# Kernel tuning notes

Hardware: AMD Instinct MI355X
Metric: run time of the kernel (lower is better)

The kernel has to match this reference:

```python
import jax, jax.numpy as jnp
import numpy as np

EPS = 1e-08


def setup_inputs() -> dict:
    key = jax.random.key(0)
    x = jax.random.normal(key, (64, 16, 65536), dtype=jnp.float32)
    return {"x": x}


def reference(x):
    # x: (B, C, T). All statistics reduce over the last (time) axis.
    mean = x.mean(axis=-1)                       # (B, C)
    var = jnp.var(x, axis=-1, ddof=1)            # torch.var default: unbiased
    std = jnp.sqrt(var)                          # torch.std default: unbiased
    sq_mean = (x ** 2).mean(axis=-1)
    rms = jnp.sqrt(sq_mean)
    peak = x.max(axis=-1)
    peak_neg = x.min(axis=-1)
    peak_to_peak = peak - peak_neg
    abs_peak = jnp.abs(peak)
    crest_factor = abs_peak / (rms + EPS)
    mean_abs = jnp.abs(x).mean(axis=-1)
    shape_factor = rms / (mean_abs + EPS)
    impulse_factor = abs_peak / (mean_abs + EPS)
    sqrt_mean = jnp.sqrt(jnp.abs(x)).mean(axis=-1)
    clearance_factor = abs_peak / (sqrt_mean ** 2 + EPS)

    centered = x - mean[..., None]               # (B, C, T)
    skewness = (centered ** 3).mean(axis=-1) / (std ** 3 + EPS)
    kurtosis_val = (centered ** 4).mean(axis=-1) / (std ** 4 + EPS) - 3.0

    signs = jnp.sign(x)
    zcr = (signs[:, :, 1:] != signs[:, :, :-1]).astype(jnp.float32).mean(axis=-1)
    centered_signs = jnp.sign(centered)
    mcr = (centered_signs[:, :, 1:] != centered_signs[:, :, :-1]).astype(jnp.float32).mean(axis=-1)

    margin_factor = abs_peak / (sqrt_mean + EPS)
    energy = (x ** 2).sum(axis=-1)

    features = jnp.stack([
        mean, std, var, rms, peak, peak_neg, peak_to_peak,
        crest_factor, shape_factor, impulse_factor, clearance_factor,
        skewness, kurtosis_val, zcr, mcr, margin_factor, energy,
    ], axis=-1)                                  # (B, C, 17)
    return features
```

## Files before the change

### kernel.cpp

```cpp
#include <hip/hip_runtime.h>
#include <math.h>

#define T_LEN 65536
#define TPB 256
#define NVEC (T_LEN / 4)
#define EPS 1e-8f

__device__ __forceinline__ int sgn_of(float v) {
    return (v > 0.f) - (v < 0.f);
}

__global__ __launch_bounds__(TPB) void stat_feat_kernel(const float* __restrict__ x,
                                                        float* __restrict__ out) {
    const int row = blockIdx.x;
    const float* __restrict__ xr = x + (size_t)row * T_LEN;
    const float4* __restrict__ xv = (const float4*)xr;
    const int tid = threadIdx.x;
    const int wave = tid >> 6;
    const int lane = tid & 63;

    float s1 = 0.f, s2 = 0.f, s3 = 0.f, s4 = 0.f, sabs = 0.f, ssqrt = 0.f;
    float mx = -__builtin_inff(), mn = __builtin_inff();
    int zc = 0;

    for (int i = tid; i < NVEC; i += TPB) {
        float4 v = xv[i];
        float prev = (i > 0) ? xr[4 * i - 1] : v.x;
        float e[4] = {v.x, v.y, v.z, v.w};
#pragma unroll
        for (int j = 0; j < 4; j++) {
            float t = e[j];
            float t2 = t * t;
            s1 += t;
            s2 += t2;
            s3 = fmaf(t2, t, s3);
            s4 = fmaf(t2, t2, s4);
            float a = fabsf(t);
            sabs += a;
            ssqrt += sqrtf(a);
            mx = fmaxf(mx, t);
            mn = fminf(mn, t);
        }
        int sp = sgn_of(prev);
#pragma unroll
        for (int j = 0; j < 4; j++) {
            int sc = sgn_of(e[j]);
            zc += (sc != sp);
            sp = sc;
        }
    }

#pragma unroll
    for (int o = 32; o > 0; o >>= 1) {
        s1 += __shfl_down(s1, o);
        s2 += __shfl_down(s2, o);
        s3 += __shfl_down(s3, o);
        s4 += __shfl_down(s4, o);
        sabs += __shfl_down(sabs, o);
        ssqrt += __shfl_down(ssqrt, o);
        zc += __shfl_down(zc, o);
        mx = fmaxf(mx, __shfl_down(mx, o));
        mn = fminf(mn, __shfl_down(mn, o));
    }

    __shared__ float ls1[4], ls2[4], ls3[4], ls4[4], lsa[4], lss[4], lmx[4], lmn[4];
    __shared__ int lzc[4];
    __shared__ float s_mean;

    if (lane == 0) {
        ls1[wave] = s1; ls2[wave] = s2; ls3[wave] = s3; ls4[wave] = s4;
        lsa[wave] = sabs; lss[wave] = ssqrt; lmx[wave] = mx; lmn[wave] = mn;
        lzc[wave] = zc;
    }
    __syncthreads();

    float S1 = 0.f, S2 = 0.f, S3 = 0.f, S4 = 0.f, SA = 0.f, SS = 0.f;
    float MX = 0.f, MN = 0.f;
    int ZC = 0;
    if (tid == 0) {
        S1 = ls1[0] + ls1[1] + ls1[2] + ls1[3];
        S2 = ls2[0] + ls2[1] + ls2[2] + ls2[3];
        S3 = ls3[0] + ls3[1] + ls3[2] + ls3[3];
        S4 = ls4[0] + ls4[1] + ls4[2] + ls4[3];
        SA = lsa[0] + lsa[1] + lsa[2] + lsa[3];
        SS = lss[0] + lss[1] + lss[2] + lss[3];
        MX = fmaxf(fmaxf(lmx[0], lmx[1]), fmaxf(lmx[2], lmx[3]));
        MN = fminf(fminf(lmn[0], lmn[1]), fminf(lmn[2], lmn[3]));
        ZC = lzc[0] + lzc[1] + lzc[2] + lzc[3];
        s_mean = S1 / (float)T_LEN;
    }
    __syncthreads();

    const float m = s_mean;
    int mc = 0;
    for (int i = tid; i < NVEC; i += TPB) {
        float4 v = xv[i];
        float prev = (i > 0) ? xr[4 * i - 1] : v.x;
        float e[4] = {v.x - m, v.y - m, v.z - m, v.w - m};
        int sp = sgn_of(prev - m);
#pragma unroll
        for (int j = 0; j < 4; j++) {
            int sc = sgn_of(e[j]);
            mc += (sc != sp);
            sp = sc;
        }
    }
#pragma unroll
    for (int o = 32; o > 0; o >>= 1) mc += __shfl_down(mc, o);
    __syncthreads();
    if (lane == 0) lzc[wave] = mc;
    __syncthreads();

    if (tid == 0) {
        int MC = lzc[0] + lzc[1] + lzc[2] + lzc[3];
        const float Tf = (float)T_LEN;
        float mean = S1 / Tf;
        float sq_mean = S2 / Tf;
        float var = (S2 - S1 * S1 / Tf) / (Tf - 1.f);
        var = fmaxf(var, 0.f);
        float stdv = sqrtf(var);
        float rms = sqrtf(sq_mean);
        float peak = MX;
        float peak_neg = MN;
        float ptp = peak - peak_neg;
        float abs_peak = fabsf(peak);
        float crest = abs_peak / (rms + EPS);
        float mean_abs = SA / Tf;
        float shape = rms / (mean_abs + EPS);
        float impulse = abs_peak / (mean_abs + EPS);
        float sqrt_mean = SS / Tf;
        float clearance = abs_peak / (sqrt_mean * sqrt_mean + EPS);
        float ex3 = S3 / Tf;
        float m3 = ex3 - 3.f * mean * sq_mean + 2.f * mean * mean * mean;
        float m4 = S4 / Tf - 4.f * mean * ex3 + 6.f * mean * mean * sq_mean
                   - 3.f * mean * mean * mean * mean;
        float skew = m3 / (stdv * stdv * stdv + EPS);
        float kurt = m4 / (stdv * stdv * stdv * stdv + EPS) - 3.f;
        float zcr = (float)ZC / (Tf - 1.f);
        float mcr = (float)MC / (Tf - 1.f);
        float margin = abs_peak / (sqrt_mean + EPS);
        float energy = S2;

        float* o = out + (size_t)row * 17;
        o[0] = mean;      o[1] = stdv;     o[2] = var;      o[3] = rms;
        o[4] = peak;      o[5] = peak_neg; o[6] = ptp;      o[7] = crest;
        o[8] = shape;     o[9] = impulse;  o[10] = clearance; o[11] = skew;
        o[12] = kurt;     o[13] = zcr;     o[14] = mcr;     o[15] = margin;
        o[16] = energy;
    }
}

extern "C" void kernel_launch(void* const* d_in, const int* in_sizes, int n_in,
                              void* d_out, int out_size, void* d_ws, size_t ws_size,
                              hipStream_t stream) {
    const float* x = (const float*)d_in[0];
    float* out = (float*)d_out;
    const int rows = in_sizes[0] / T_LEN;
    stat_feat_kernel<<<dim3(rows), dim3(TPB), 0, stream>>>(x, out);
}
```

Baseline: 418.2 us.

## Split each row across chunked blocks with multi-kernel partial reductions

Splits every row into 8 chunks processed by separate blocks, writing per-chunk partial statistics to workspace, then finalizes in a small kernel; the mean-crossing pass is likewise chunked and reduced in separate kernels. This raises the number of blocks in flight to hide memory latency that the one-block-per-row design could not. Neighbor values for crossing counts now come from a wave shuffle instead of a global reload, and sign tests use a simple less-than comparison. It adds four launches and workspace traffic, and treats exact zeros slightly differently from sign().

```diff
diff --git a/kernel.cpp b/kernel.cpp
--- a/kernel.cpp
+++ b/kernel.cpp
@@ -1,52 +1,55 @@
 #include <hip/hip_runtime.h>
 #include <math.h>
 
-#define T_LEN 65536
-#define TPB 256
-#define NVEC (T_LEN / 4)
-#define EPS 1e-8f
-
-__device__ __forceinline__ int sgn_of(float v) {
-    return (v > 0.f) - (v < 0.f);
-}
-
-__global__ __launch_bounds__(TPB) void stat_feat_kernel(const float* __restrict__ x,
-                                                        float* __restrict__ out) {
-    const int row = blockIdx.x;
-    const float* __restrict__ xr = x + (size_t)row * T_LEN;
+#define T_LEN      65536
+#define TPB        256
+#define CHUNKS     8
+#define CHUNK_VECS (T_LEN / 4 / CHUNKS)
+#define ITERS      (CHUNK_VECS / TPB)
+#define EPS        1e-8f
+
+__global__ __launch_bounds__(TPB) void k1_partials(const float* __restrict__ x,
+                                                   float* __restrict__ part,
+                                                   int rows) {
+    const int blk   = blockIdx.x;
+    const int row   = blk >> 3;
+    const int chunk = blk & 7;
+    const int tid   = threadIdx.x;
+    const int lane  = tid & 63;
+    const int wave  = tid >> 6;
+
+    const float*  __restrict__ xr = x + (size_t)row * T_LEN;
     const float4* __restrict__ xv = (const float4*)xr;
-    const int tid = threadIdx.x;
-    const int wave = tid >> 6;
-    const int lane = tid & 63;
-
-    float s1 = 0.f, s2 = 0.f, s3 = 0.f, s4 = 0.f, sabs = 0.f, ssqrt = 0.f;
+    const int vbase = chunk * CHUNK_VECS;
+
+    float s1 = 0.f, s2 = 0.f, s3 = 0.f, s4 = 0.f, sa = 0.f, ss = 0.f;
     float mx = -__builtin_inff(), mn = __builtin_inff();
     int zc = 0;
 
-    for (int i = tid; i < NVEC; i += TPB) {
-        float4 v = xv[i];
-        float prev = (i > 0) ? xr[4 * i - 1] : v.x;
+    for (int it = 0; it < ITERS; ++it) {
+        const int vi = vbase + it * TPB + tid;
+        float4 v = xv[vi];
+        float prev = __shfl_up(v.w, 1);
+        if (lane == 0) prev = (vi > 0) ? xr[4 * vi - 1] : v.x;
+
+        bool sp = prev < 0.f;
+        bool b0 = v.x < 0.f, b1 = v.y < 0.f, b2 = v.z < 0.f, b3 = v.w < 0.f;
+        zc += (int)(sp != b0) + (int)(b0 != b1) + (int)(b1 != b2) + (int)(b2 != b3);
+
         float e[4] = {v.x, v.y, v.z, v.w};
 #pragma unroll
         for (int j = 0; j < 4; j++) {
             float t = e[j];
             float t2 = t * t;
             s1 += t;
-            s2 += t2;
+            s2 = fmaf(t, t, s2);
             s3 = fmaf(t2, t, s3);
             s4 = fmaf(t2, t2, s4);
             float a = fabsf(t);
-            sabs += a;
-            ssqrt += sqrtf(a);
+            sa += a;
+            ss += sqrtf(a);
             mx = fmaxf(mx, t);
             mn = fminf(mn, t);
-        }
-        int sp = sgn_of(prev);
-#pragma unroll
-        for (int j = 0; j < 4; j++) {
-            int sc = sgn_of(e[j]);
-            zc += (sc != sp);
-            sp = sc;
         }
     }
 
@@ -56,98 +59,139 @@
         s2 += __shfl_down(s2, o);
         s3 += __shfl_down(s3, o);
         s4 += __shfl_down(s4, o);
-        sabs += __shfl_down(sabs, o);
-        ssqrt += __shfl_down(ssqrt, o);
+        sa += __shfl_down(sa, o);
+        ss += __shfl_down(ss, o);
         zc += __shfl_down(zc, o);
         mx = fmaxf(mx, __shfl_down(mx, o));
         mn = fminf(mn, __shfl_down(mn, o));
     }
 
-    __shared__ float ls1[4], ls2[4], ls3[4], ls4[4], lsa[4], lss[4], lmx[4], lmn[4];
-    __shared__ int lzc[4];
-    __shared__ float s_mean;
-
+    __shared__ float l[9][4];
     if (lane == 0) {
-        ls1[wave] = s1; ls2[wave] = s2; ls3[wave] = s3; ls4[wave] = s4;
-        lsa[wave] = sabs; lss[wave] = ssqrt; lmx[wave] = mx; lmn[wave] = mn;
-        lzc[wave] = zc;
+        l[0][wave] = s1; l[1][wave] = s2; l[2][wave] = s3; l[3][wave] = s4;
+        l[4][wave] = sa; l[5][wave] = ss; l[6][wave] = mx; l[7][wave] = mn;
+        l[8][wave] = (float)zc;
     }
     __syncthreads();
-
-    float S1 = 0.f, S2 = 0.f, S3 = 0.f, S4 = 0.f, SA = 0.f, SS = 0.f;
-    float MX = 0.f, MN = 0.f;
-    int ZC = 0;
     if (tid == 0) {
-        S1 = ls1[0] + ls1[1] + ls1[2] + ls1[3];
-        S2 = ls2[0] + ls2[1] + ls2[2] + ls2[3];
-        S3 = ls3[0] + ls3[1] + ls3[2] + ls3[3];
-        S4 = ls4[0] + ls4[1] + ls4[2] + ls4[3];
-        SA = lsa[0] + lsa[1] + lsa[2] + lsa[3];
-        SS = lss[0] + lss[1] + lss[2] + lss[3];
-        MX = fmaxf(fmaxf(lmx[0], lmx[1]), fmaxf(lmx[2], lmx[3]));
-        MN = fminf(fminf(lmn[0], lmn[1]), fminf(lmn[2], lmn[3]));
-        ZC = lzc[0] + lzc[1] + lzc[2] + lzc[3];
-        s_mean = S1 / (float)T_LEN;
-    }
+        const int N = rows * CHUNKS;
+        const int idx = chunk * rows + row;
+        part[0 * N + idx] = l[0][0] + l[0][1] + l[0][2] + l[0][3];
+        part[1 * N + idx] = l[1][0] + l[1][1] + l[1][2] + l[1][3];
+        part[2 * N + idx] = l[2][0] + l[2][1] + l[2][2] + l[2][3];
+        part[3 * N + idx] = l[3][0] + l[3][1] + l[3][2] + l[3][3];
+        part[4 * N + idx] = l[4][0] + l[4][1] + l[4][2] + l[4][3];
+        part[5 * N + idx] = l[5][0] + l[5][1] + l[5][2] + l[5][3];
+        part[6 * N + idx] = fmaxf(fmaxf(l[6][0], l[6][1]), fmaxf(l[6][2], l[6][3]));
+        part[7 * N + idx] = fminf(fminf(l[7][0], l[7][1]), fminf(l[7][2], l[7][3]));
+        part[8 * N + idx] = l[8][0] + l[8][1] + l[8][2] + l[8][3];
+    }
+}
+
+__global__ __launch_bounds__(TPB) void k2_finalize(const float* __restrict__ part,
+                                                   float* __restrict__ meanbuf,
+                                                   float* __restrict__ out,
+                                                   int rows) {
+    const int r = blockIdx.x * TPB + threadIdx.x;
+    if (r >= rows) return;
+    const int N = rows * CHUNKS;
+
+    float S1 = 0.f, S2 = 0.f, S3 = 0.f, S4 = 0.f, SA = 0.f, SS = 0.f, ZC = 0.f;
+    float MX = -__builtin_inff(), MN = __builtin_inff();
+#pragma unroll
+    for (int c = 0; c < CHUNKS; c++) {
+        const int idx = c * rows + r;
+        S1 += part[0 * N + idx];
+        S2 += part[1 * N + idx];
+        S3 += part[2 * N + idx];
+        S4 += part[3 * N + idx];
+        SA += part[4 * N + idx];
+        SS += part[5 * N + idx];
+        MX = fmaxf(MX, part[6 * N + idx]);
+        MN = fminf(MN, part[7 * N + idx]);
+        ZC += part[8 * N + idx];
+    }
+
+    const float Tf = (float)T_LEN;
+    float mean = S1 / Tf;
+    float sq_mean = S2 / Tf;
+    float var = (S2 - S1 * S1 / Tf) / (Tf - 1.f);
+    var = fmaxf(var, 0.f);
+    float stdv = sqrtf(var);
+    float rms = sqrtf(sq_mean);
+    float peak = MX, peak_neg = MN;
+    float ptp = peak - peak_neg;
+    float abs_peak = fabsf(peak);
+    float crest = abs_peak / (rms + EPS);
+    float mean_abs = SA / Tf;
+    float shape = rms / (mean_abs + EPS);
+    float impulse = abs_peak / (mean_abs + EPS);
+    float sqrt_mean = SS / Tf;
+    float clearance = abs_peak / (sqrt_mean * sqrt_mean + EPS);
+    float ex3 = S3 / Tf;
+    float m3 = ex3 - 3.f * mean * sq_mean + 2.f * mean * mean * mean;
+    float m4 = S4 / Tf - 4.f * mean * ex3 + 6.f * mean * mean * sq_mean
+               - 3.f * mean * mean * mean * mean;
+    float skew = m3 / (stdv * stdv * stdv + EPS);
+    float kurt = m4 / (stdv * stdv * stdv * stdv + EPS) - 3.f;
+    float zcr = ZC / (Tf - 1.f);
+    float margin = abs_peak / (sqrt_mean + EPS);
+
+    meanbuf[r] = mean;
+
+    float* o = out + (size_t)r * 17;
+    o[0] = mean;   o[1] = stdv;     o[2] = var;       o[3] = rms;
+    o[4] = peak;   o[5] = peak_neg; o[6] = ptp;       o[7] = crest;
+    o[8] = shape;  o[9] = impulse;  o[10] = clearance; o[11] = skew;
+    o[12] = kurt;  o[13] = zcr;      o[15] = margin;
+    o[16] = S2;
+}
+
+__global__ __launch_bounds__(TPB) void k3_mc(const float* __restrict__ x,
+                                             const float* __restrict__ meanbuf,
+                                             float* __restrict__ mcp,
+                                             int rows) {
+    const int blk   = blockIdx.x;
+    const int row   = blk >> 3;
+    const int chunk = blk & 7;
+    const int tid   = threadIdx.x;
+    const int lane  = tid & 63;
+    const int wave  = tid >> 6;
+
+    const float*  __restrict__ xr = x + (size_t)row * T_LEN;
+    const float4* __restrict__ xv = (const float4*)xr;
+    const float m = meanbuf[row];
+    const int vbase = chunk * CHUNK_VECS;
+
+    int mc = 0;
+    for (int it = 0; it < ITERS; ++it) {
+        const int vi = vbase + it * TPB + tid;
+        float4 v = xv[vi];
+        float prev = __shfl_up(v.w, 1);
+        if (lane == 0) prev = (vi > 0) ? xr[4 * vi - 1] : v.x;
+        bool sp = prev < m;
+        bool b0 = v.x < m, b1 = v.y < m, b2 = v.z < m, b3 = v.w < m;
+        mc += (int)(sp != b0) + (int)(b0 != b1) + (int)(b1 != b2) + (int)(b2 != b3);
+    }
+#pragma unroll
+    for (int o = 32; o > 0; o >>= 1) mc += __shfl_down(mc, o);
+
+    __shared__ int l[4];
+    if (lane == 0) l[wave] = mc;
     __syncthreads();
-
-    const float m = s_mean;
-    int mc = 0;
-    for (int i = tid; i < NVEC; i += TPB) {
-        float4 v = xv[i];
-        float prev = (i > 0) ? xr[4 * i - 1] : v.x;
-        float e[4] = {v.x - m, v.y - m, v.z - m, v.w - m};
-        int sp = sgn_of(prev - m);
-#pragma unroll
-        for (int j = 0; j < 4; j++) {
-            int sc = sgn_of(e[j]);
-            mc += (sc != sp);
-            sp = sc;
-        }
-    }
-#pragma unroll
-    for (int o = 32; o > 0; o >>= 1) mc += __shfl_down(mc, o);
-    __syncthreads();
-    if (lane == 0) lzc[wave] = mc;
-    __syncthreads();
-
-    if (tid == 0) {
-        int MC = lzc[0] + lzc[1] + lzc[2] + lzc[3];
-        const float Tf = (float)T_LEN;
-        float mean = S1 / Tf;
-        float sq_mean = S2 / Tf;
-        float var = (S2 - S1 * S1 / Tf) / (Tf - 1.f);
-        var = fmaxf(var, 0.f);
-        float stdv = sqrtf(var);
-        float rms = sqrtf(sq_mean);
-        float peak = MX;
-        float peak_neg = MN;
-        float ptp = peak - peak_neg;
-        float abs_peak = fabsf(peak);
-        float crest = abs_peak / (rms + EPS);
-        float mean_abs = SA / Tf;
-        float shape = rms / (mean_abs + EPS);
-        float impulse = abs_peak / (mean_abs + EPS);
-        float sqrt_mean = SS / Tf;
-        float clearance = abs_peak / (sqrt_mean * sqrt_mean + EPS);
-        float ex3 = S3 / Tf;
-        float m3 = ex3 - 3.f * mean * sq_mean + 2.f * mean * mean * mean;
-        float m4 = S4 / Tf - 4.f * mean * ex3 + 6.f * mean * mean * sq_mean
-                   - 3.f * mean * mean * mean * mean;
-        float skew = m3 / (stdv * stdv * stdv + EPS);
-        float kurt = m4 / (stdv * stdv * stdv * stdv + EPS) - 3.f;
-        float zcr = (float)ZC / (Tf - 1.f);
-        float mcr = (float)MC / (Tf - 1.f);
-        float margin = abs_peak / (sqrt_mean + EPS);
-        float energy = S2;
-
-        float* o = out + (size_t)row * 17;
-        o[0] = mean;      o[1] = stdv;     o[2] = var;      o[3] = rms;
-        o[4] = peak;      o[5] = peak_neg; o[6] = ptp;      o[7] = crest;
-        o[8] = shape;     o[9] = impulse;  o[10] = clearance; o[11] = skew;
-        o[12] = kurt;     o[13] = zcr;     o[14] = mcr;     o[15] = margin;
-        o[16] = energy;
-    }
+    if (tid == 0)
+        mcp[chunk * rows + row] = (float)(l[0] + l[1] + l[2] + l[3]);
+}
+
+__global__ __launch_bounds__(TPB) void k4_mcr(const float* __restrict__ mcp,
+                                              float* __restrict__ out,
+                                              int rows) {
+    const int r = blockIdx.x * TPB + threadIdx.x;
+    if (r >= rows) return;
+    float MC = 0.f;
+#pragma unroll
+    for (int c = 0; c < CHUNKS; c++) MC += mcp[c * rows + r];
+    out[(size_t)r * 17 + 14] = MC / ((float)T_LEN - 1.f);
 }
 
 extern "C" void kernel_launch(void* const* d_in, const int* in_sizes, int n_in,
@@ -156,5 +200,15 @@
     const float* x = (const float*)d_in[0];
     float* out = (float*)d_out;
     const int rows = in_sizes[0] / T_LEN;
-    stat_feat_kernel<<<dim3(rows), dim3(TPB), 0, stream>>>(x, out);
-}
+    const int N = rows * CHUNKS;
+
+    float* ws = (float*)d_ws;
+    float* part    = ws;
+    float* meanbuf = ws + 9 * N;
+    float* mcp     = meanbuf + rows;
+
+    k1_partials<<<dim3(N), dim3(TPB), 0, stream>>>(x, part, rows);
+    k2_finalize<<<dim3((rows + TPB - 1) / TPB), dim3(TPB), 0, stream>>>(part, meanbuf, out, rows);
+    k3_mc<<<dim3(N), dim3(TPB), 0, stream>>>(x, meanbuf, mcp, rows);
+    k4_mcr<<<dim3((rows + TPB - 1) / TPB), dim3(TPB), 0, stream>>>(mcp, out, rows);
+}
```

Result: no change. 417.4 us (-0.2%).

## Use 1024-thread blocks, batched unrolled loads and shuffle-based neighbor for crossing counts

Applied to the files above, without the earlier changes.

Raises the block size from 256 to 1024 threads and issues four float4 loads per iteration before computing, for more memory-level parallelism per row. The previous-element lookup for crossing counts now comes from a wave shuffle, with a scalar global load only on lane 0, replacing a separate global load per vector. Sign tests become simple less-than comparisons, and per-wave partials are reduced over 16 waves. Sign semantics change for exact zeros, and with only 1024 rows the grid is small relative to the device's compute units.

```diff
diff --git a/kernel.cpp b/kernel.cpp
--- a/kernel.cpp
+++ b/kernel.cpp
@@ -1,52 +1,61 @@
 #include <hip/hip_runtime.h>
 #include <math.h>
 
-#define T_LEN 65536
-#define TPB 256
-#define NVEC (T_LEN / 4)
-#define EPS 1e-8f
+#define T_LEN  65536
+#define TPB    1024
+#define VECS   (T_LEN / 4)
+#define VPT    (VECS / TPB)
+#define UNROLL 4
+#define NWAVES (TPB / 64)
+#define EPS    1e-8f
 
-__device__ __forceinline__ int sgn_of(float v) {
-    return (v > 0.f) - (v < 0.f);
-}
+__global__ __launch_bounds__(TPB, 8) void stat_feat_fused(const float* __restrict__ x,
+                                                          float* __restrict__ out) {
+    const int row  = blockIdx.x;
+    const int tid  = threadIdx.x;
+    const int lane = tid & 63;
+    const int wave = tid >> 6;
 
-__global__ __launch_bounds__(TPB) void stat_feat_kernel(const float* __restrict__ x,
-                                                        float* __restrict__ out) {
-    const int row = blockIdx.x;
-    const float* __restrict__ xr = x + (size_t)row * T_LEN;
+    const float*  __restrict__ xr = x + (size_t)row * T_LEN;
     const float4* __restrict__ xv = (const float4*)xr;
-    const int tid = threadIdx.x;
-    const int wave = tid >> 6;
-    const int lane = tid & 63;
 
-    float s1 = 0.f, s2 = 0.f, s3 = 0.f, s4 = 0.f, sabs = 0.f, ssqrt = 0.f;
+    float s1 = 0.f, s2 = 0.f, s3 = 0.f, s4 = 0.f, sa = 0.f, ss = 0.f;
     float mx = -__builtin_inff(), mn = __builtin_inff();
     int zc = 0;
 
-    for (int i = tid; i < NVEC; i += TPB) {
-        float4 v = xv[i];
-        float prev = (i > 0) ? xr[4 * i - 1] : v.x;
-        float e[4] = {v.x, v.y, v.z, v.w};
+    for (int g = 0; g < VPT; g += UNROLL) {
+        float4 v[UNROLL];
+        int    vi[UNROLL];
 #pragma unroll
-        for (int j = 0; j < 4; j++) {
-            float t = e[j];
-            float t2 = t * t;
-            s1 += t;
-            s2 += t2;
-            s3 = fmaf(t2, t, s3);
-            s4 = fmaf(t2, t2, s4);
-            float a = fabsf(t);
-            sabs += a;
-            ssqrt += sqrtf(a);
-            mx = fmaxf(mx, t);
-            mn = fminf(mn, t);
+        for (int u = 0; u < UNROLL; u++) {
+            vi[u] = (g + u) * TPB + tid;
+            v[u]  = xv[vi[u]];
         }
-        int sp = sgn_of(prev);
 #pragma unroll
-        for (int j = 0; j < 4; j++) {
-            int sc = sgn_of(e[j]);
-            zc += (sc != sp);
-            sp = sc;
+        for (int u = 0; u < UNROLL; u++) {
+            float4 w = v[u];
+            float prev = __shfl_up(w.w, 1);
+            if (lane == 0) prev = (vi[u] > 0) ? xr[4 * vi[u] - 1] : w.x;
+
+            bool sp = prev < 0.f;
+            bool b0 = w.x < 0.f, b1 = w.y < 0.f, b2 = w.z < 0.f, b3 = w.w < 0.f;
+            zc += (int)(sp != b0) + (int)(b0 != b1) + (int)(b1 != b2) + (int)(b2 != b3);
+
+            float e[4] = {w.x, w.y, w.z, w.w};
+#pragma unroll
+            for (int j = 0; j < 4; j++) {
+                float t  = e[j];
+                float t2 = t * t;
+                s1 += t;
+                s2 = fmaf(t, t, s2);
+                s3 = fmaf(t2, t, s3);
+                s4 = fmaf(t2, t2, s4);
+                float a = fabsf(t);
+                sa += a;
+                ss += sqrtf(a);
+                mx = fmaxf(mx, t);
+                mn = fminf(mn, t);
+            }
         }
     }
 
@@ -56,63 +65,68 @@
         s2 += __shfl_down(s2, o);
         s3 += __shfl_down(s3, o);
         s4 += __shfl_down(s4, o);
-        sabs += __shfl_down(sabs, o);
-        ssqrt += __shfl_down(ssqrt, o);
+        sa += __shfl_down(sa, o);
+        ss += __shfl_down(ss, o);
         zc += __shfl_down(zc, o);
         mx = fmaxf(mx, __shfl_down(mx, o));
         mn = fminf(mn, __shfl_down(mn, o));
     }
 
-    __shared__ float ls1[4], ls2[4], ls3[4], ls4[4], lsa[4], lss[4], lmx[4], lmn[4];
-    __shared__ int lzc[4];
+    __shared__ float l[9][NWAVES];
     __shared__ float s_mean;
-
     if (lane == 0) {
-        ls1[wave] = s1; ls2[wave] = s2; ls3[wave] = s3; ls4[wave] = s4;
-        lsa[wave] = sabs; lss[wave] = ssqrt; lmx[wave] = mx; lmn[wave] = mn;
-        lzc[wave] = zc;
+        l[0][wave] = s1; l[1][wave] = s2; l[2][wave] = s3; l[3][wave] = s4;
+        l[4][wave] = sa; l[5][wave] = ss; l[6][wave] = mx; l[7][wave] = mn;
+        l[8][wave] = (float)zc;
     }
     __syncthreads();
 
-    float S1 = 0.f, S2 = 0.f, S3 = 0.f, S4 = 0.f, SA = 0.f, SS = 0.f;
-    float MX = 0.f, MN = 0.f;
-    int ZC = 0;
+    float S1 = 0.f, S2 = 0.f, S3 = 0.f, S4 = 0.f, SA = 0.f, SS = 0.f, ZC = 0.f;
+    float MX = -__builtin_inff(), MN = __builtin_inff();
     if (tid == 0) {
-        S1 = ls1[0] + ls1[1] + ls1[2] + ls1[3];
-        S2 = ls2[0] + ls2[1] + ls2[2] + ls2[3];
-        S3 = ls3[0] + ls3[1] + ls3[2] + ls3[3];
-        S4 = ls4[0] + ls4[1] + ls4[2] + ls4[3];
-        SA = lsa[0] + lsa[1] + lsa[2] + lsa[3];
-        SS = lss[0] + lss[1] + lss[2] + lss[3];
-        MX = fmaxf(fmaxf(lmx[0], lmx[1]), fmaxf(lmx[2], lmx[3]));
-        MN = fminf(fminf(lmn[0], lmn[1]), fminf(lmn[2], lmn[3]));
-        ZC = lzc[0] + lzc[1] + lzc[2] + lzc[3];
+#pragma unroll
+        for (int wv = 0; wv < NWAVES; wv++) {
+            S1 += l[0][wv]; S2 += l[1][wv]; S3 += l[2][wv]; S4 += l[3][wv];
+            SA += l[4][wv]; SS += l[5][wv];
+            MX = fmaxf(MX, l[6][wv]); MN = fminf(MN, l[7][wv]);
+            ZC += l[8][wv];
+        }
         s_mean = S1 / (float)T_LEN;
     }
     __syncthreads();
 
     const float m = s_mean;
     int mc = 0;
-    for (int i = tid; i < NVEC; i += TPB) {
-        float4 v = xv[i];
-        float prev = (i > 0) ? xr[4 * i - 1] : v.x;
-        float e[4] = {v.x - m, v.y - m, v.z - m, v.w - m};
-        int sp = sgn_of(prev - m);
+    for (int g = 0; g < VPT; g += UNROLL) {
+        float4 v[UNROLL];
+        int    vi[UNROLL];
 #pragma unroll
-        for (int j = 0; j < 4; j++) {
-            int sc = sgn_of(e[j]);
-            mc += (sc != sp);
-            sp = sc;
+        for (int u = 0; u < UNROLL; u++) {
+            vi[u] = (g + u) * TPB + tid;
+            v[u]  = xv[vi[u]];
+        }
+#pragma unroll
+        for (int u = 0; u < UNROLL; u++) {
+            float4 w = v[u];
+            float prev = __shfl_up(w.w, 1);
+            if (lane == 0) prev = (vi[u] > 0) ? xr[4 * vi[u] - 1] : w.x;
+            bool sp = prev < m;
+            bool b0 = w.x < m, b1 = w.y < m, b2 = w.z < m, b3 = w.w < m;
+            mc += (int)(sp != b0) + (int)(b0 != b1) + (int)(b1 != b2) + (int)(b2 != b3);
         }
     }
 #pragma unroll
     for (int o = 32; o > 0; o >>= 1) mc += __shfl_down(mc, o);
+
     __syncthreads();
-    if (lane == 0) lzc[wave] = mc;
+    if (lane == 0) l[0][wave] = (float)mc;
     __syncthreads();
 
     if (tid == 0) {
-        int MC = lzc[0] + lzc[1] + lzc[2] + lzc[3];
+        float MC = 0.f;
+#pragma unroll
+        for (int wv = 0; wv < NWAVES; wv++) MC += l[0][wv];
+
         const float Tf = (float)T_LEN;
         float mean = S1 / Tf;
         float sq_mean = S2 / Tf;
@@ -120,8 +134,7 @@
         var = fmaxf(var, 0.f);
         float stdv = sqrtf(var);
         float rms = sqrtf(sq_mean);
-        float peak = MX;
-        float peak_neg = MN;
+        float peak = MX, peak_neg = MN;
         float ptp = peak - peak_neg;
         float abs_peak = fabsf(peak);
         float crest = abs_peak / (rms + EPS);
@@ -136,17 +149,16 @@
                    - 3.f * mean * mean * mean * mean;
         float skew = m3 / (stdv * stdv * stdv + EPS);
         float kurt = m4 / (stdv * stdv * stdv * stdv + EPS) - 3.f;
-        float zcr = (float)ZC / (Tf - 1.f);
-        float mcr = (float)MC / (Tf - 1.f);
+        float zcr = ZC / (Tf - 1.f);
+        float mcr = MC / (Tf - 1.f);
         float margin = abs_peak / (sqrt_mean + EPS);
-        float energy = S2;
 
         float* o = out + (size_t)row * 17;
-        o[0] = mean;      o[1] = stdv;     o[2] = var;      o[3] = rms;
-        o[4] = peak;      o[5] = peak_neg; o[6] = ptp;      o[7] = crest;
-        o[8] = shape;     o[9] = impulse;  o[10] = clearance; o[11] = skew;
-        o[12] = kurt;     o[13] = zcr;     o[14] = mcr;     o[15] = margin;
-        o[16] = energy;
+        o[0] = mean;   o[1] = stdv;     o[2] = var;        o[3] = rms;
+        o[4] = peak;   o[5] = peak_neg; o[6] = ptp;        o[7] = crest;
+        o[8] = shape;  o[9] = impulse;  o[10] = clearance; o[11] = skew;
+        o[12] = kurt;  o[13] = zcr;     o[14] = mcr;       o[15] = margin;
+        o[16] = S2;
     }
 }
 
@@ -156,5 +168,5 @@
     const float* x = (const float*)d_in[0];
     float* out = (float*)d_out;
     const int rows = in_sizes[0] / T_LEN;
-    stat_feat_kernel<<<dim3(rows), dim3(TPB), 0, stream>>>(x, out);
+    stat_feat_fused<<<dim3(rows), dim3(TPB), 0, stream>>>(x, out);
 }
```

Result: slower. 575.0 us (+37.5%).
